# Optimization experiments

Hardware: AMD Instinct MI355X
Metric: run time of the kernel (lower is better)

Reference implementation:

```python
import jax, jax.numpy as jnp
import numpy as np

N_NODES = 100000
N_EDGES = 200000
N_GRAPHS = 4096
NODE_DIM = 64
HID = 256
N_GAT = 4
NEG_SLOPE = 0.2
EPS = 1e-9


def setup_inputs() -> dict:
    key = jax.random.key(0)
    ks = jax.random.split(key, 16)
    node_feats = jax.random.normal(ks[0], (N_NODES, NODE_DIM), dtype=jnp.float32)
    src = jax.random.randint(ks[1], (N_EDGES,), 0, N_NODES)
    dst = jax.random.randint(ks[2], (N_EDGES,), 0, N_NODES)
    graph_ids = jnp.sort(jax.random.randint(ks[3], (N_NODES,), 0, N_GRAPHS))
    s = 1.0 / np.sqrt(HID)
    w_embed = jax.random.normal(ks[4], (NODE_DIM, HID), dtype=jnp.float32) / np.sqrt(NODE_DIM)
    b_embed = jnp.zeros((HID,), dtype=jnp.float32)
    gat_W = jax.random.normal(ks[5], (N_GAT, HID, HID), dtype=jnp.float32) * s
    gat_al = jax.random.normal(ks[6], (N_GAT, HID), dtype=jnp.float32) * s
    gat_ar = jax.random.normal(ks[7], (N_GAT, HID), dtype=jnp.float32) * s
    w1 = jax.random.normal(ks[8], (HID, HID // 2), dtype=jnp.float32) * s
    b1 = jnp.zeros((HID // 2,), dtype=jnp.float32)
    w2 = jax.random.normal(ks[9], (HID // 2, HID // 4), dtype=jnp.float32) / np.sqrt(HID // 2)
    b2 = jnp.zeros((HID // 4,), dtype=jnp.float32)
    w3 = jax.random.normal(ks[10], (HID // 4, 1), dtype=jnp.float32) / np.sqrt(HID // 4)
    b3 = jnp.zeros((1,), dtype=jnp.float32)
    return dict(node_feats=node_feats, src=src, dst=dst, graph_ids=graph_ids,
                w_embed=w_embed, b_embed=b_embed, gat_W=gat_W, gat_al=gat_al,
                gat_ar=gat_ar, w1=w1, b1=b1, w2=w2, b2=b2, w3=w3, b3=b3)


def _gat_layer(h, W, al, ar, src, dst):
    z = h @ W                                   # [N, HID]
    el = z @ al                                 # [N] source attention term
    er = z @ ar                                 # [N] destination attention term
    e = jax.nn.leaky_relu(el[src] + er[dst], NEG_SLOPE)   # [E]
    # segment softmax over edges grouped by destination node
    emax = jax.ops.segment_max(e, dst, num_segments=N_NODES)
    emax = jnp.where(jnp.isfinite(emax), emax, 0.0)
    ex = jnp.exp(e - emax[dst])
    esum = jax.ops.segment_sum(ex, dst, num_segments=N_NODES)
    alpha = ex / (esum[dst] + EPS)              # [E]
    m = jax.ops.segment_sum(alpha[:, None] * z[src], dst, num_segments=N_NODES)
    return jax.nn.relu(m + h)                   # residual + ReLU


def reference(node_feats, src, dst, graph_ids, w_embed, b_embed,
              gat_W, gat_al, gat_ar, w1, b1, w2, b2, w3, b3):
    h = node_feats @ w_embed + b_embed          # node embedding
    for l in range(N_GAT):
        h = _gat_layer(h, gat_W[l], gat_al[l], gat_ar[l], src, dst)
    g = jax.ops.segment_sum(h, graph_ids, num_segments=N_GRAPHS)  # sum pooling [G, HID]
    g = jax.nn.relu(g @ w1 + b1)
    g = jax.nn.relu(g @ w2 + b2)
    return g @ w3 + b3                          # [G, 1]
```

## Files before the change

kernel.cpp:

```cpp
#include <hip/hip_runtime.h>
#include <hip/hip_bf16.h>

#define N_NODES 100000
#define N_EDGES 200000
#define N_GRAPHS 4096
#define NODE_DIM 64
#define HID 256
#define N_GAT 4
#define NEG_SLOPE 0.2f
#define EPS 1e-9f
#define NB 98

typedef const __attribute__((address_space(1))) void gv_t;
typedef __attribute__((address_space(3))) void lv_t;
typedef __attribute__((ext_vector_type(8))) short bf16x8;
typedef __attribute__((ext_vector_type(4))) float f32x4;

__device__ __forceinline__ float b2f(unsigned short u) {
    return __uint_as_float(((unsigned)u) << 16);
}
__device__ __forceinline__ unsigned short f2b(float f) {
    unsigned u = __float_as_uint(f);
    return (unsigned short)((u + 0x7fffu + ((u >> 16) & 1u)) >> 16);
}

__global__ void convert_f32_bf16(const float* __restrict__ src,
                                 unsigned short* __restrict__ dst, int n4) {
    int i = blockIdx.x * 256 + threadIdx.x;
    if (i >= n4) return;
    float4 v = ((const float4*)src)[i];
    ushort4 o;
    o.x = f2b(v.x); o.y = f2b(v.y); o.z = f2b(v.z); o.w = f2b(v.w);
    ((ushort4*)dst)[i] = o;
}

__global__ __launch_bounds__(256) void transpose_bf16(const float* __restrict__ W,
                                                      unsigned short* __restrict__ Wt,
                                                      int K) {
    __shared__ float tile[32][33];
    const int kb = blockIdx.x * 32, cb = blockIdx.y * 32;
    const int tr = threadIdx.x >> 5, tc = threadIdx.x & 31;
#pragma unroll
    for (int i = 0; i < 4; ++i)
        tile[tr + i * 8][tc] = W[(size_t)(kb + tr + i * 8) * HID + cb + tc];
    __syncthreads();
#pragma unroll
    for (int i = 0; i < 4; ++i)
        Wt[(size_t)(cb + tr + i * 8) * K + kb + tc] = f2b(tile[tc][tr + i * 8]);
}

template <int K, bool BIAS, bool DOTS>
__global__ __launch_bounds__(256) void gemm_mfma(const unsigned short* __restrict__ Xb,
                                                 const unsigned short* __restrict__ Wt,
                                                 const float* __restrict__ bias,
                                                 unsigned short* __restrict__ Yb,
                                                 const float* __restrict__ al,
                                                 const float* __restrict__ ar,
                                                 float* __restrict__ el,
                                                 float* __restrict__ er,
                                                 int M) {
    constexpr int KC = 64;
    __shared__ unsigned short xs[128 * KC];
    __shared__ unsigned short wsx[128 * KC];
    const int t = threadIdx.x, wv = t >> 6, ln = t & 63;
    const int wr2 = wv >> 1, wc2 = wv & 1;
    const long row0 = (long)blockIdx.x * 128;
    const int  col0 = blockIdx.y * 128;

    f32x4 acc[4][4];
#pragma unroll
    for (int m = 0; m < 4; ++m)
#pragma unroll
        for (int n = 0; n < 4; ++n) acc[m][n] = (f32x4){0.f, 0.f, 0.f, 0.f};

    for (int k0 = 0; k0 < K; k0 += KC) {
#pragma unroll
        for (int i = 0; i < 4; ++i) {
            const int chunk = wv * 4 + i;
            const int row = chunk * 8 + (ln >> 3);
            const int gsrc = (ln & 7) ^ (row & 7);
            long gr = row0 + row; if (gr >= M) gr = M - 1;
            const unsigned short* gp = Xb + gr * K + k0 + gsrc * 8;
            __builtin_amdgcn_global_load_lds((gv_t*)gp, (lv_t*)(xs + chunk * 512 + ln * 8), 16, 0, 0);
        }
#pragma unroll
        for (int i = 0; i < 4; ++i) {
            const int chunk = wv * 4 + i;
            const int row = chunk * 8 + (ln >> 3);
            const int gsrc = (ln & 7) ^ (row & 7);
            const unsigned short* gp = Wt + (size_t)(col0 + row) * K + k0 + gsrc * 8;
            __builtin_amdgcn_global_load_lds((gv_t*)gp, (lv_t*)(wsx + chunk * 512 + ln * 8), 16, 0, 0);
        }
        __syncthreads();

#pragma unroll
        for (int kk = 0; kk < 2; ++kk) {
            bf16x8 a[4], b[4];
            const int g = kk * 4 + (ln >> 4);
#pragma unroll
            for (int m = 0; m < 4; ++m) {
                const int row = wr2 * 64 + m * 16 + (ln & 15);
                const int s = g ^ (row & 7);
                a[m] = *(const bf16x8*)&xs[row * 64 + s * 8];
            }
#pragma unroll
            for (int n = 0; n < 4; ++n) {
                const int row = wc2 * 64 + n * 16 + (ln & 15);
                const int s = g ^ (row & 7);
                b[n] = *(const bf16x8*)&wsx[row * 64 + s * 8];
            }
#pragma unroll
            for (int m = 0; m < 4; ++m)
#pragma unroll
                for (int n = 0; n < 4; ++n)
                    acc[m][n] = __builtin_amdgcn_mfma_f32_16x16x32_bf16(a[m], b[n], acc[m][n], 0, 0, 0);
        }
        __syncthreads();
    }

    float bj[4];
#pragma unroll
    for (int n = 0; n < 4; ++n)
        bj[n] = BIAS ? bias[col0 + wc2 * 64 + n * 16 + (ln & 15)] : 0.f;

#pragma unroll
    for (int m = 0; m < 4; ++m) {
        const long rbase = row0 + wr2 * 64 + m * 16 + 4 * (ln >> 4);
#pragma unroll
        for (int n = 0; n < 4; ++n) {
            const int col = col0 + wc2 * 64 + n * 16 + (ln & 15);
#pragma unroll
            for (int q = 0; q < 4; ++q) {
                const long r = rbase + q;
                if (r >= M) continue;
                Yb[r * HID + col] = f2b(acc[m][n][q] + bj[n]);
            }
        }
    }

    if (DOTS) {
        float alv[4], arv[4];
#pragma unroll
        for (int n = 0; n < 4; ++n) {
            const int col = col0 + wc2 * 64 + n * 16 + (ln & 15);
            alv[n] = al[col];
            arv[n] = ar[col];
        }
#pragma unroll
        for (int m = 0; m < 4; ++m) {
#pragma unroll
            for (int q = 0; q < 4; ++q) {
                float pl = 0.f, pr = 0.f;
#pragma unroll
                for (int n = 0; n < 4; ++n) {
                    pl = fmaf(acc[m][n][q], alv[n], pl);
                    pr = fmaf(acc[m][n][q], arv[n], pr);
                }
#pragma unroll
                for (int o = 1; o < 16; o <<= 1) {
                    pl += __shfl_xor(pl, o);
                    pr += __shfl_xor(pr, o);
                }
                if ((ln & 15) == 0) {
                    const long r = row0 + wr2 * 64 + m * 16 + 4 * (ln >> 4) + q;
                    if (r < M) {
                        atomicAdd(&el[r], pl);
                        atomicAdd(&er[r], pr);
                    }
                }
            }
        }
    }
}

__global__ void hist_dst(const int* __restrict__ dst, int* __restrict__ deg) {
    int i = blockIdx.x * 256 + threadIdx.x;
    if (i < N_EDGES) atomicAdd(&deg[dst[i]], 1);
}

__global__ __launch_bounds__(1024) void scan_block(const int* __restrict__ deg,
                                                   int* __restrict__ sexc,
                                                   int* __restrict__ bsum) {
    int t = threadIdx.x, gid = blockIdx.x * 1024 + t;
    int v = (gid < N_NODES) ? deg[gid] : 0;
    int lane = t & 63, wv = t >> 6;
    int x = v;
#pragma unroll
    for (int o = 1; o < 64; o <<= 1) {
        int y = __shfl_up(x, o);
        if (lane >= o) x += y;
    }
    __shared__ int wsum[16];
    if (lane == 63) wsum[wv] = x;
    __syncthreads();
    if (t == 0) {
        int a = 0;
#pragma unroll
        for (int i = 0; i < 16; ++i) { int tt = wsum[i]; wsum[i] = a; a += tt; }
        bsum[blockIdx.x] = a;
    }
    __syncthreads();
    sexc[gid] = (x - v) + wsum[wv];
}

__global__ __launch_bounds__(128) void scan_partials(int* __restrict__ bsum,
                                                     int* __restrict__ offsets) {
    __shared__ int s[128];
    int t = threadIdx.x;
    int v = (t < NB) ? bsum[t] : 0;
    s[t] = v;
    __syncthreads();
    for (int o = 1; o < 128; o <<= 1) {
        int y = (t >= o) ? s[t - o] : 0;
        __syncthreads();
        s[t] += y;
        __syncthreads();
    }
    if (t < NB) bsum[t] = s[t] - v;
    if (t == 127) offsets[N_NODES] = s[127];
}

__global__ __launch_bounds__(1024) void scan_add(const int* __restrict__ sexc,
                                                 const int* __restrict__ bsum,
                                                 int* __restrict__ offsets) {
    int gid = blockIdx.x * 1024 + threadIdx.x;
    if (gid < N_NODES) offsets[gid] = sexc[gid] + bsum[blockIdx.x];
}

__global__ void csr_fill(const int* __restrict__ src, const int* __restrict__ dst,
                         const int* __restrict__ offsets, int* __restrict__ cnt,
                         int* __restrict__ csrc) {
    int i = blockIdx.x * 256 + threadIdx.x;
    if (i < N_EDGES) {
        int d = dst[i];
        int slot = offsets[d] + atomicAdd(&cnt[d], 1);
        csrc[slot] = src[i];
    }
}

__global__ void graph_offsets(const int* __restrict__ gid, int* __restrict__ goff) {
    int g = blockIdx.x * 256 + threadIdx.x;
    if (g > N_GRAPHS) return;
    int lo = 0, hi = N_NODES;
    while (lo < hi) {
        int mid = (lo + hi) >> 1;
        if (gid[mid] < g) lo = mid + 1; else hi = mid;
    }
    goff[g] = lo;
}

__global__ __launch_bounds__(256) void alpha_kernel(const int* __restrict__ offs,
                                                    const int* __restrict__ csrc,
                                                    const float* __restrict__ el,
                                                    const float* __restrict__ er,
                                                    float* __restrict__ alpha) {
    int n = blockIdx.x * 256 + threadIdx.x;
    if (n >= N_NODES) return;
    const int beg = offs[n], end = offs[n + 1];
    if (beg == end) return;
    const float ern = er[n];
    float m = -3.4e38f;
    for (int c = beg; c < end; ++c) {
        float v = el[csrc[c]] + ern;
        v = (v >= 0.f) ? v : NEG_SLOPE * v;
        alpha[c] = v;
        m = fmaxf(m, v);
    }
    float s = 0.f;
    for (int c = beg; c < end; ++c) {
        float a = __expf(alpha[c] - m);
        alpha[c] = a;
        s += a;
    }
    const float inv = 1.f / (s + EPS);
    for (int c = beg; c < end; ++c) alpha[c] *= inv;
}

__global__ __launch_bounds__(256) void gather_attn(const int* __restrict__ offs,
                                                   const int* __restrict__ csrc,
                                                   const float* __restrict__ alpha,
                                                   const unsigned short* __restrict__ z,
                                                   unsigned short* __restrict__ Ab) {
    const int n = blockIdx.x * 4 + (threadIdx.x >> 6);
    const int lane = threadIdx.x & 63;
    const int beg = offs[n], end = offs[n + 1];

    float4 acc = make_float4(0.f, 0.f, 0.f, 0.f);
    for (int c = beg; c < end; ++c) {
        float a = alpha[c];
        int sc = csrc[c];
        ushort4 zz = ((const ushort4*)(z + (size_t)sc * HID))[lane];
        acc.x = fmaf(a, b2f(zz.x), acc.x);
        acc.y = fmaf(a, b2f(zz.y), acc.y);
        acc.z = fmaf(a, b2f(zz.z), acc.z);
        acc.w = fmaf(a, b2f(zz.w), acc.w);
    }

    ushort4* Ap = (ushort4*)(Ab + (size_t)n * HID);
    ushort4 hh = Ap[lane];
    ushort4 ob;
    ob.x = f2b(fmaxf(b2f(hh.x) + acc.x, 0.f));
    ob.y = f2b(fmaxf(b2f(hh.y) + acc.y, 0.f));
    ob.z = f2b(fmaxf(b2f(hh.z) + acc.z, 0.f));
    ob.w = f2b(fmaxf(b2f(hh.w) + acc.w, 0.f));
    Ap[lane] = ob;
}

__global__ __launch_bounds__(256) void pool_seg(const unsigned short* __restrict__ h,
                                                const int* __restrict__ goff,
                                                float* __restrict__ g) {
    const int gi = blockIdx.x, t = threadIdx.x;
    const int beg = goff[gi], end = goff[gi + 1];
    float acc = 0.f;
    for (int n = beg; n < end; ++n) acc += b2f(h[(size_t)n * HID + t]);
    g[(size_t)gi * HID + t] = acc;
}

__global__ void mlp_kernel(const float* __restrict__ g,
                           const float* __restrict__ w1, const float* __restrict__ b1,
                           const float* __restrict__ w2, const float* __restrict__ b2,
                           const float* __restrict__ w3, const float* __restrict__ b3,
                           float* __restrict__ out) {
    int gi = blockIdx.x, t = threadIdx.x;
    __shared__ float x[HID];
    __shared__ float y1[HID / 2];
    __shared__ float y2[HID / 4];
    x[t] = g[gi * HID + t];
    __syncthreads();
    if (t < HID / 2) {
        float a = b1[t];
#pragma unroll 8
        for (int k = 0; k < HID; ++k) a += x[k] * w1[k * (HID / 2) + t];
        y1[t] = fmaxf(a, 0.f);
    }
    __syncthreads();
    if (t < HID / 4) {
        float a = b2[t];
#pragma unroll 8
        for (int k = 0; k < HID / 2; ++k) a += y1[k] * w2[k * (HID / 4) + t];
        y2[t] = fmaxf(a, 0.f);
    }
    __syncthreads();
    if (t < 64) {
        float p = y2[t] * w3[t];
#pragma unroll
        for (int off = 32; off > 0; off >>= 1) p += __shfl_down(p, off);
        if (t == 0) out[gi] = p + b3[0];
    }
}

extern "C" void kernel_launch(void* const* d_in, const int* in_sizes, int n_in,
                              void* d_out, int out_size, void* d_ws, size_t ws_size,
                              hipStream_t stream) {
    const float* node_feats = (const float*)d_in[0];
    const int*   src        = (const int*)d_in[1];
    const int*   dst        = (const int*)d_in[2];
    const int*   graph_ids  = (const int*)d_in[3];
    const float* w_embed    = (const float*)d_in[4];
    const float* b_embed    = (const float*)d_in[5];
    const float* gat_W      = (const float*)d_in[6];
    const float* gat_al     = (const float*)d_in[7];
    const float* gat_ar     = (const float*)d_in[8];
    const float* w1         = (const float*)d_in[9];
    const float* b1         = (const float*)d_in[10];
    const float* w2         = (const float*)d_in[11];
    const float* b2         = (const float*)d_in[12];
    const float* w3         = (const float*)d_in[13];
    const float* b3         = (const float*)d_in[14];
    float* out = (float*)d_out;

    char* ws = (char*)d_ws;
    size_t off = 0;
    auto alloc = [&](size_t bytes) { char* p = ws + off; off += (bytes + 255) & ~size_t(255); return p; };
    unsigned short* Ab      = (unsigned short*)alloc((size_t)N_NODES * HID * 2);
    unsigned short* Zb      = (unsigned short*)alloc((size_t)N_NODES * HID * 2);
    unsigned short* Wt      = (unsigned short*)alloc((size_t)HID * HID * 2);
    float*          eler    = (float*)alloc((size_t)2 * N_NODES * 4);
    float*          alpha   = (float*)alloc((size_t)N_EDGES * 4);
    int*            deg     = (int*)alloc((size_t)N_NODES * 4);
    int*            cnt     = (int*)alloc((size_t)N_NODES * 4);
    int*            sexc    = (int*)alloc((size_t)NB * 1024 * 4);
    int*            bsum    = (int*)alloc(128 * 4);
    int*            offsets = (int*)alloc((size_t)(N_NODES + 1) * 4);
    int*            csrc    = (int*)alloc((size_t)N_EDGES * 4);
    int*            goff    = (int*)alloc((size_t)(N_GRAPHS + 1) * 4);
    float*          g       = (float*)alloc((size_t)N_GRAPHS * HID * 4);
    float*          el      = eler;
    float*          er      = eler + N_NODES;
    unsigned short* nfb     = Zb;

    hipMemsetAsync(deg, 0, (size_t)N_NODES * 4, stream);
    hipMemsetAsync(cnt, 0, (size_t)N_NODES * 4, stream);
    hist_dst<<<(N_EDGES + 255) / 256, 256, 0, stream>>>(dst, deg);
    scan_block<<<NB, 1024, 0, stream>>>(deg, sexc, bsum);
    scan_partials<<<1, 128, 0, stream>>>(bsum, offsets);
    scan_add<<<NB, 1024, 0, stream>>>(sexc, bsum, offsets);
    csr_fill<<<(N_EDGES + 255) / 256, 256, 0, stream>>>(src, dst, offsets, cnt, csrc);
    graph_offsets<<<(N_GRAPHS + 256) / 256, 256, 0, stream>>>(graph_ids, goff);

    dim3 ggrid((N_NODES + 127) / 128, HID / 128);

    convert_f32_bf16<<<(N_NODES * NODE_DIM / 4 + 255) / 256, 256, 0, stream>>>(node_feats, nfb, N_NODES * NODE_DIM / 4);
    transpose_bf16<<<dim3(NODE_DIM / 32, HID / 32), 256, 0, stream>>>(w_embed, Wt, NODE_DIM);
    gemm_mfma<NODE_DIM, true, false><<<ggrid, 256, 0, stream>>>(
        nfb, Wt, b_embed, Ab, nullptr, nullptr, nullptr, nullptr, N_NODES);

    for (int l = 0; l < N_GAT; ++l) {
        const float* W  = gat_W  + (size_t)l * HID * HID;
        const float* al = gat_al + (size_t)l * HID;
        const float* ar = gat_ar + (size_t)l * HID;

        transpose_bf16<<<dim3(HID / 32, HID / 32), 256, 0, stream>>>(W, Wt, HID);
        hipMemsetAsync(eler, 0, (size_t)2 * N_NODES * 4, stream);
        gemm_mfma<HID, false, true><<<ggrid, 256, 0, stream>>>(
            Ab, Wt, nullptr, Zb, al, ar, el, er, N_NODES);
        alpha_kernel<<<(N_NODES + 255) / 256, 256, 0, stream>>>(offsets, csrc, el, er, alpha);
        gather_attn<<<N_NODES / 4, 256, 0, stream>>>(offsets, csrc, alpha, Zb, Ab);
    }

    pool_seg<<<N_GRAPHS, 256, 0, stream>>>(Ab, goff, g);
    mlp_kernel<<<N_GRAPHS, HID, 0, stream>>>(g, w1, b1, w2, b2, w3, b3, out);
}
```

Baseline: 522.7 us.

## Double-buffer GEMM LDS tiles, init CSR cursors in scan, unroll gather

The MFMA GEMM now uses two LDS buffers and prefetches the next K-chunk while computing the current one. This is meant to hide global-to-LDS load latency behind the matrix math, at the cost of twice the shared memory per block. The CSR build now seeds its per-node cursor array directly with the scanned offsets. That removes a memset and one offsets read per edge in csr_fill. The attention gather loop is unrolled by two so two neighbor rows are loaded at once, raising memory-level parallelism.

```diff
diff --git a/kernel.cpp b/kernel.cpp
--- a/kernel.cpp
+++ b/kernel.cpp
@@ -60,20 +60,15 @@
                                                  float* __restrict__ er,
                                                  int M) {
     constexpr int KC = 64;
-    __shared__ unsigned short xs[128 * KC];
-    __shared__ unsigned short wsx[128 * KC];
+    constexpr int NT = K / KC;
+    __shared__ unsigned short xs[2][128 * KC];
+    __shared__ unsigned short wsx[2][128 * KC];
     const int t = threadIdx.x, wv = t >> 6, ln = t & 63;
     const int wr2 = wv >> 1, wc2 = wv & 1;
     const long row0 = (long)blockIdx.x * 128;
     const int  col0 = blockIdx.y * 128;
 
-    f32x4 acc[4][4];
-#pragma unroll
-    for (int m = 0; m < 4; ++m)
-#pragma unroll
-        for (int n = 0; n < 4; ++n) acc[m][n] = (f32x4){0.f, 0.f, 0.f, 0.f};
-
-    for (int k0 = 0; k0 < K; k0 += KC) {
+    auto stage = [&](int buf, int k0) {
 #pragma unroll
         for (int i = 0; i < 4; ++i) {
             const int chunk = wv * 4 + i;
@@ -81,7 +76,7 @@
             const int gsrc = (ln & 7) ^ (row & 7);
             long gr = row0 + row; if (gr >= M) gr = M - 1;
             const unsigned short* gp = Xb + gr * K + k0 + gsrc * 8;
-            __builtin_amdgcn_global_load_lds((gv_t*)gp, (lv_t*)(xs + chunk * 512 + ln * 8), 16, 0, 0);
+            __builtin_amdgcn_global_load_lds((gv_t*)gp, (lv_t*)(&xs[buf][chunk * 512 + ln * 8]), 16, 0, 0);
         }
 #pragma unroll
         for (int i = 0; i < 4; ++i) {
@@ -89,9 +84,23 @@
             const int row = chunk * 8 + (ln >> 3);
             const int gsrc = (ln & 7) ^ (row & 7);
             const unsigned short* gp = Wt + (size_t)(col0 + row) * K + k0 + gsrc * 8;
-            __builtin_amdgcn_global_load_lds((gv_t*)gp, (lv_t*)(wsx + chunk * 512 + ln * 8), 16, 0, 0);
-        }
-        __syncthreads();
+            __builtin_amdgcn_global_load_lds((gv_t*)gp, (lv_t*)(&wsx[buf][chunk * 512 + ln * 8]), 16, 0, 0);
+        }
+    };
+
+    f32x4 acc[4][4];
+#pragma unroll
+    for (int m = 0; m < 4; ++m)
+#pragma unroll
+        for (int n = 0; n < 4; ++n) acc[m][n] = (f32x4){0.f, 0.f, 0.f, 0.f};
+
+    stage(0, 0);
+    __syncthreads();
+
+#pragma unroll
+    for (int tt = 0; tt < NT; ++tt) {
+        const int cur = tt & 1;
+        if (tt + 1 < NT) stage(cur ^ 1, (tt + 1) * KC);
 
 #pragma unroll
         for (int kk = 0; kk < 2; ++kk) {
@@ -101,13 +110,13 @@
             for (int m = 0; m < 4; ++m) {
                 const int row = wr2 * 64 + m * 16 + (ln & 15);
                 const int s = g ^ (row & 7);
-                a[m] = *(const bf16x8*)&xs[row * 64 + s * 8];
+                a[m] = *(const bf16x8*)&xs[cur][row * 64 + s * 8];
             }
 #pragma unroll
             for (int n = 0; n < 4; ++n) {
                 const int row = wc2 * 64 + n * 16 + (ln & 15);
                 const int s = g ^ (row & 7);
-                b[n] = *(const bf16x8*)&wsx[row * 64 + s * 8];
+                b[n] = *(const bf16x8*)&wsx[cur][row * 64 + s * 8];
             }
 #pragma unroll
             for (int m = 0; m < 4; ++m)
@@ -222,18 +231,21 @@
 
 __global__ __launch_bounds__(1024) void scan_add(const int* __restrict__ sexc,
                                                  const int* __restrict__ bsum,
-                                                 int* __restrict__ offsets) {
+                                                 int* __restrict__ offsets,
+                                                 int* __restrict__ cnt) {
     int gid = blockIdx.x * 1024 + threadIdx.x;
-    if (gid < N_NODES) offsets[gid] = sexc[gid] + bsum[blockIdx.x];
+    if (gid < N_NODES) {
+        int v = sexc[gid] + bsum[blockIdx.x];
+        offsets[gid] = v;
+        cnt[gid] = v;
+    }
 }
 
 __global__ void csr_fill(const int* __restrict__ src, const int* __restrict__ dst,
-                         const int* __restrict__ offsets, int* __restrict__ cnt,
-                         int* __restrict__ csrc) {
+                         int* __restrict__ cnt, int* __restrict__ csrc) {
     int i = blockIdx.x * 256 + threadIdx.x;
     if (i < N_EDGES) {
-        int d = dst[i];
-        int slot = offsets[d] + atomicAdd(&cnt[d], 1);
+        int slot = atomicAdd(&cnt[dst[i]], 1);
         csrc[slot] = src[i];
     }
 }
@@ -286,7 +298,18 @@
     const int beg = offs[n], end = offs[n + 1];
 
     float4 acc = make_float4(0.f, 0.f, 0.f, 0.f);
-    for (int c = beg; c < end; ++c) {
+    int c = beg;
+    for (; c + 1 < end; c += 2) {
+        float a0 = alpha[c], a1 = alpha[c + 1];
+        int s0 = csrc[c], s1 = csrc[c + 1];
+        ushort4 z0 = ((const ushort4*)(z + (size_t)s0 * HID))[lane];
+        ushort4 z1 = ((const ushort4*)(z + (size_t)s1 * HID))[lane];
+        acc.x = fmaf(a0, b2f(z0.x), acc.x); acc.x = fmaf(a1, b2f(z1.x), acc.x);
+        acc.y = fmaf(a0, b2f(z0.y), acc.y); acc.y = fmaf(a1, b2f(z1.y), acc.y);
+        acc.z = fmaf(a0, b2f(z0.z), acc.z); acc.z = fmaf(a1, b2f(z1.z), acc.z);
+        acc.w = fmaf(a0, b2f(z0.w), acc.w); acc.w = fmaf(a1, b2f(z1.w), acc.w);
+    }
+    if (c < end) {
         float a = alpha[c];
         int sc = csrc[c];
         ushort4 zz = ((const ushort4*)(z + (size_t)sc * HID))[lane];
@@ -390,12 +413,11 @@
     unsigned short* nfb     = Zb;
 
     hipMemsetAsync(deg, 0, (size_t)N_NODES * 4, stream);
-    hipMemsetAsync(cnt, 0, (size_t)N_NODES * 4, stream);
     hist_dst<<<(N_EDGES + 255) / 256, 256, 0, stream>>>(dst, deg);
     scan_block<<<NB, 1024, 0, stream>>>(deg, sexc, bsum);
     scan_partials<<<1, 128, 0, stream>>>(bsum, offsets);
-    scan_add<<<NB, 1024, 0, stream>>>(sexc, bsum, offsets);
-    csr_fill<<<(N_EDGES + 255) / 256, 256, 0, stream>>>(src, dst, offsets, cnt, csrc);
+    scan_add<<<NB, 1024, 0, stream>>>(sexc, bsum, offsets, cnt);
+    csr_fill<<<(N_EDGES + 255) / 256, 256, 0, stream>>>(src, dst, cnt, csrc);
     graph_offsets<<<(N_GRAPHS + 256) / 256, 256, 0, stream>>>(graph_ids, goff);
 
     dim3 ggrid((N_NODES + 127) / 128, HID / 128);
```

After: 510.7 us. 1.02x faster.
